# Optimization experiments

Hardware: AMD Instinct MI355X
Metric: run time of the kernel (lower is better)

## Reference

```python
import jax, jax.numpy as jnp
import numpy as np

N = 768
C_IN = 128
C_OUT = 64
C_DGRAM = 39
C_AA = 22
C_ESM = 1280
LN_EPS = 1e-5


def _layer_norm(x, g, b):
    mu = jnp.mean(x, axis=-1, keepdims=True)
    var = jnp.var(x, axis=-1, keepdims=True)
    return (x - mu) * jax.lax.rsqrt(var + LN_EPS) * g + b


def setup_inputs() -> dict:
    key = jax.random.key(0)
    ks = jax.random.split(key, 36)
    rn = lambda k, s, sc=1.0: jax.random.normal(k, s, dtype=jnp.float32) * sc
    ru = lambda k, s: jax.random.uniform(k, s, dtype=jnp.float32)
    w = lambda k, cin: rn(k, (cin, C_OUT), 1.0 / np.sqrt(cin))
    z = jnp.zeros((C_OUT,), jnp.float32)
    return {
        "template_dgram": rn(ks[0], (N, N, C_DGRAM)),
        "aatype_one_hot": ru(ks[1], (N, C_AA)),
        "query_embedding": rn(ks[2], (N, N, C_IN)),
        "pseudo_beta_mask": ru(ks[3], (N,)),
        "backbone_mask": ru(ks[4], (N,)),
        "multichain_mask_2d": ru(ks[5], (N, N)),
        "unit_x": rn(ks[6], (N, N)),
        "unit_y": rn(ks[7], (N, N)),
        "unit_z": rn(ks[8], (N, N)),
        "esm_embedding": rn(ks[9], (N, C_ESM)),
        "w_dgram": w(ks[10], C_DGRAM), "b_dgram": z,
        "w_aa1": w(ks[11], C_AA), "b_aa1": z,
        "w_aa2": w(ks[12], C_AA), "b_aa2": z,
        "ln_g": jnp.ones((C_IN,), jnp.float32), "ln_b": jnp.zeros((C_IN,), jnp.float32),
        "w_q": w(ks[13], C_IN), "b_q": z,
        "w_pbm": w(ks[14], 1), "b_pbm": z,
        "w_x": w(ks[15], 1), "b_x": z,
        "w_y": w(ks[16], 1), "b_y": z,
        "w_z": w(ks[17], 1), "b_z": z,
        "w_bb": w(ks[18], 1), "b_bb": z,
        "w_esm1": w(ks[19], C_ESM), "b_esm1": z,
        "w_esm2": w(ks[20], C_ESM), "b_esm2": z,
    }


def reference(template_dgram, aatype_one_hot, query_embedding, pseudo_beta_mask,
              backbone_mask, multichain_mask_2d, unit_x, unit_y, unit_z, esm_embedding,
              w_dgram, b_dgram, w_aa1, b_aa1, w_aa2, b_aa2, ln_g, ln_b, w_q, b_q,
              w_pbm, b_pbm, w_x, b_x, w_y, b_y, w_z, b_z, w_bb, b_bb,
              w_esm1, b_esm1, w_esm2, b_esm2):
    # pair masks [N, N]
    pb2 = pseudo_beta_mask[:, None] * pseudo_beta_mask[None, :] * multichain_mask_2d
    bb2 = backbone_mask[:, None] * backbone_mask[None, :] * multichain_mask_2d
    # masked distogram -> GEMM over bins
    act = jnp.einsum('ijd,do->ijo', template_dgram * bb2[..., None], w_dgram) + b_dgram
    # Linear(1, c_out) branches: scalar * weight row + bias (broadcasts)
    act = act + (pb2[..., None] * w_pbm[0] + b_pbm)
    # per-residue aatype projections broadcast over rows / columns
    act = act + (aatype_one_hot @ w_aa1 + b_aa1)[None, :, :]
    act = act + (aatype_one_hot @ w_aa2 + b_aa2)[:, None, :]
    act = act + ((unit_x * bb2)[..., None] * w_x[0] + b_x)
    act = act + ((unit_y * bb2)[..., None] * w_y[0] + b_y)
    act = act + ((unit_z * bb2)[..., None] * w_z[0] + b_z)
    act = act + (bb2[..., None] * w_bb[0] + b_bb)
    # per-residue ESM projections broadcast over rows / columns
    act = act + (esm_embedding @ w_esm1 + b_esm1)[None, :, :]
    act = act + (esm_embedding @ w_esm2 + b_esm2)[:, None, :]
    # LayerNorm + projection of the query pair embedding [N, N, c_in]
    q = _layer_norm(query_embedding, ln_g, ln_b)
    act = act + jnp.einsum('ijc,co->ijo', q, w_q) + b_q
    return act
```

## Files before the change

kernel.cpp:

```cpp
#include <hip/hip_runtime.h>

#define NN 768
#define CIN 128
#define COUT 64
#define CDG 39
#define CAA 22
#define CESM 1280

typedef __attribute__((ext_vector_type(8))) short short8;
typedef __attribute__((ext_vector_type(4))) float f32x4;

__device__ __forceinline__ unsigned short f2bf(float f) {
  union { float f; unsigned int i; } c; c.f = f;
  unsigned int u = c.i;
  u += 0x7fffu + ((u >> 16) & 1u);
  return (unsigned short)(u >> 16);
}
__device__ __forceinline__ unsigned int pk(float a, float b) {
  return (unsigned int)f2bf(a) | ((unsigned int)f2bf(b) << 16);
}

struct Args {
  const float *td, *aa, *q, *pbm, *bbm, *mc, *ux, *uy, *uz, *esm;
  const float *w_dgram, *b_dgram, *w_aa1, *b_aa1, *w_aa2, *b_aa2;
  const float *ln_g, *ln_b, *w_q, *b_q;
  const float *w_pbm, *b_pbm, *w_x, *b_x, *w_y, *b_y, *w_z, *b_z, *w_bb, *b_bb;
  const float *w_esm1, *b_esm1, *w_esm2, *b_esm2;
  float* out;
  float* row_vec; float* col_vec; unsigned short* b_pack;
};

__global__ __launch_bounds__(256) void k_pre(Args a) {
  const int b = blockIdx.x;
  const int tid = threadIdx.x;
  if (b == NN) {
    for (int e = tid; e < 12288; e += 256) {
      int jj = e & 7;
      int lane = (e >> 3) & 63;
      int qt = e >> 9;
      int q = qt >> 2, t = qt & 3;
      int k = q * 32 + ((lane >> 4) << 3) + jj;
      int n = t * 16 + (lane & 15);
      float v = 0.f;
      if (k < CIN) v = a.ln_g[k] * a.w_q[k * COUT + n];
      else if (k < CIN + CDG) v = a.w_dgram[(k - CIN) * COUT + n];
      else if (k == 167) v = a.w_pbm[n];
      else if (k == 168) v = a.w_x[n];
      else if (k == 169) v = a.w_y[n];
      else if (k == 170) v = a.w_z[n];
      else if (k == 171) v = a.w_bb[n];
      a.b_pack[e] = f2bf(v);
    }
    return;
  }
  const int wv = tid >> 6, lane = tid & 63;
  float acc1 = 0.f, acc2 = 0.f;
  const int KT = CAA + CESM;
  const int SL = (KT + 3) / 4;
  int k0 = wv * SL;
  int k1 = k0 + SL; if (k1 > KT) k1 = KT;
  for (int k = k0; k < k1; ++k) {
    float v; const float *w1, *w2;
    if (k < CAA) { v = a.aa[b * CAA + k]; w1 = a.w_aa1 + k * COUT; w2 = a.w_aa2 + k * COUT; }
    else { int e = k - CAA; v = a.esm[b * CESM + e]; w1 = a.w_esm1 + e * COUT; w2 = a.w_esm2 + e * COUT; }
    acc1 += v * w1[lane];
    acc2 += v * w2[lane];
  }
  __shared__ float red1[4][64];
  __shared__ float red2[4][64];
  red1[wv][lane] = acc1; red2[wv][lane] = acc2;
  __syncthreads();
  if (wv == 0) {
    float r1 = red1[0][lane] + red1[1][lane] + red1[2][lane] + red1[3][lane];
    float r2 = red2[0][lane] + red2[1][lane] + red2[2][lane] + red2[3][lane];
    float bq = 0.f;
    for (int c = 0; c < CIN; ++c) bq += a.ln_b[c] * a.w_q[c * COUT + lane];
    float br = a.b_aa1[lane] + a.b_esm1[lane] + a.b_dgram[lane] +
               a.b_pbm[lane] + a.b_x[lane] + a.b_y[lane] +
               a.b_z[lane] + a.b_bb[lane] + a.b_q[lane] + bq;
    float bc = a.b_aa2[lane] + a.b_esm2[lane];
    a.row_vec[b * COUT + lane] = r1 + br;
    a.col_vec[b * COUT + lane] = r2 + bc;
  }
}

__global__ __launch_bounds__(256, 4) void k_main(Args a) {
  const int jt = blockIdx.x;
  const int i  = blockIdx.y;
  const int jbase = jt * 64;
  const int tid = threadIdx.x;
  const int wv = tid >> 6, lane = tid & 63;
  const int m = lane & 15, quad = lane >> 4;

  __shared__ unsigned short B_lds[12288];
  __shared__ unsigned short A2[64][72];
  __shared__ float bb2_s[64];
  __shared__ float pb2_s[64];

  const float* qrow = a.q + ((size_t)i * NN + jbase + wv * 16 + m) * CIN + quad * 8;
  float4 qv[8];
#pragma unroll
  for (int qq = 0; qq < 4; ++qq) {
    qv[2 * qq]     = *(const float4*)(qrow + qq * 32);
    qv[2 * qq + 1] = *(const float4*)(qrow + qq * 32 + 4);
  }

  if (tid < 64) {
    int j = jbase + tid;
    float mc  = a.mc[(size_t)i * NN + j];
    bb2_s[tid] = a.bbm[i] * a.bbm[j] * mc;
    pb2_s[tid] = a.pbm[i] * a.pbm[j] * mc;
  }

  {
    const int4* src = (const int4*)a.b_pack;
    int4* dst = (int4*)B_lds;
#pragma unroll
    for (int r = 0; r < 6; ++r) dst[tid + 256 * r] = src[tid + 256 * r];
  }

  float sum = 0.f, sq = 0.f;
#pragma unroll
  for (int v = 0; v < 8; ++v) {
    float4 t4 = qv[v];
    sum += t4.x + t4.y + t4.z + t4.w;
    sq  += t4.x * t4.x + t4.y * t4.y + t4.z * t4.z + t4.w * t4.w;
  }
  sum += __shfl_xor(sum, 16); sum += __shfl_xor(sum, 32);
  sq  += __shfl_xor(sq, 16);  sq  += __shfl_xor(sq, 32);
  const float mu  = sum * (1.f / 128.f);
  const float var = sq * (1.f / 128.f) - mu * mu;
  const float rs  = rsqrtf(var + 1e-5f);

  short8 af[4];
#pragma unroll
  for (int qq = 0; qq < 4; ++qq) {
    union { short8 s; unsigned int w[4]; } u;
    float4 lo = qv[2 * qq], hi = qv[2 * qq + 1];
    u.w[0] = pk((lo.x - mu) * rs, (lo.y - mu) * rs);
    u.w[1] = pk((lo.z - mu) * rs, (lo.w - mu) * rs);
    u.w[2] = pk((hi.x - mu) * rs, (hi.y - mu) * rs);
    u.w[3] = pk((hi.z - mu) * rs, (hi.w - mu) * rs);
    af[qq] = u.s;
  }

  __syncthreads();

  {
    const float* base = a.td + ((size_t)i * NN + jbase) * CDG;
    const float2* src = (const float2*)base;
    for (int w = tid; w < (64 * CDG) / 2; w += 256) {
      float2 d2 = src[w];
      int f0 = w * 2;
      int p0 = (f0 * 26887) >> 20; int d0 = f0 - p0 * CDG;
      int f1 = f0 + 1;
      int p1 = (f1 * 26887) >> 20; int d1 = f1 - p1 * CDG;
      A2[p0][d0] = f2bf(d2.x * bb2_s[p0]);
      A2[p1][d1] = f2bf(d2.y * bb2_s[p1]);
    }
  }
  if (tid < 64) {
    int p = tid;
    size_t gij = (size_t)i * NN + jbase + p;
    float bb = bb2_s[p];
    A2[p][39] = f2bf(pb2_s[p]);
    A2[p][40] = f2bf(a.ux[gij] * bb);
    A2[p][41] = f2bf(a.uy[gij] * bb);
    A2[p][42] = f2bf(a.uz[gij] * bb);
    A2[p][43] = f2bf(bb);
    unsigned int* zp = (unsigned int*)&A2[p][44];
#pragma unroll
    for (int z = 0; z < 10; ++z) zp[z] = 0;
  }
  __syncthreads();

  f32x4 acc[4];
#pragma unroll
  for (int t = 0; t < 4; ++t) { f32x4 z = {0.f, 0.f, 0.f, 0.f}; acc[t] = z; }
  const unsigned short* Bb = &B_lds[lane * 8];
#pragma unroll
  for (int qq = 0; qq < 4; ++qq) {
#pragma unroll
    for (int t = 0; t < 4; ++t) {
      short8 bfr = *(const short8*)(Bb + (qq * 4 + t) * 512);
      acc[t] = __builtin_amdgcn_mfma_f32_16x16x32_bf16(af[qq], bfr, acc[t], 0, 0, 0);
    }
  }
  const unsigned short* Ab2 = &A2[wv * 16 + m][quad * 8];
#pragma unroll
  for (int q = 4; q < 6; ++q) {
    short8 a8 = *(const short8*)(Ab2 + (q - 4) * 32);
#pragma unroll
    for (int t = 0; t < 4; ++t) {
      short8 bfr = *(const short8*)(Bb + (q * 4 + t) * 512);
      acc[t] = __builtin_amdgcn_mfma_f32_16x16x32_bf16(a8, bfr, acc[t], 0, 0, 0);
    }
  }

  const float* cvp = a.col_vec + (size_t)i * COUT;
#pragma unroll
  for (int t = 0; t < 4; ++t) {
    int n = t * 16 + m;
    float cv = cvp[n];
#pragma unroll
    for (int r = 0; r < 4; ++r) {
      int p = wv * 16 + quad * 4 + r;
      int j = jbase + p;
      float val = acc[t][r] + a.row_vec[j * COUT + n] + cv;
      a.out[((size_t)i * NN + j) * COUT + n] = val;
    }
  }
}

extern "C" void kernel_launch(void* const* d_in, const int* in_sizes, int n_in,
                              void* d_out, int out_size, void* d_ws, size_t ws_size,
                              hipStream_t stream) {
  Args a;
  a.td     = (const float*)d_in[0];
  a.aa     = (const float*)d_in[1];
  a.q      = (const float*)d_in[2];
  a.pbm    = (const float*)d_in[3];
  a.bbm    = (const float*)d_in[4];
  a.mc     = (const float*)d_in[5];
  a.ux     = (const float*)d_in[6];
  a.uy     = (const float*)d_in[7];
  a.uz     = (const float*)d_in[8];
  a.esm    = (const float*)d_in[9];
  a.w_dgram = (const float*)d_in[10]; a.b_dgram = (const float*)d_in[11];
  a.w_aa1   = (const float*)d_in[12]; a.b_aa1   = (const float*)d_in[13];
  a.w_aa2   = (const float*)d_in[14]; a.b_aa2   = (const float*)d_in[15];
  a.ln_g    = (const float*)d_in[16]; a.ln_b    = (const float*)d_in[17];
  a.w_q     = (const float*)d_in[18]; a.b_q     = (const float*)d_in[19];
  a.w_pbm   = (const float*)d_in[20]; a.b_pbm   = (const float*)d_in[21];
  a.w_x     = (const float*)d_in[22]; a.b_x     = (const float*)d_in[23];
  a.w_y     = (const float*)d_in[24]; a.b_y     = (const float*)d_in[25];
  a.w_z     = (const float*)d_in[26]; a.b_z     = (const float*)d_in[27];
  a.w_bb    = (const float*)d_in[28]; a.b_bb    = (const float*)d_in[29];
  a.w_esm1  = (const float*)d_in[30]; a.b_esm1  = (const float*)d_in[31];
  a.w_esm2  = (const float*)d_in[32]; a.b_esm2  = (const float*)d_in[33];
  a.out = (float*)d_out;
  a.row_vec = (float*)d_ws;
  a.col_vec = a.row_vec + NN * COUT;
  a.b_pack  = (unsigned short*)(a.col_vec + NN * COUT);

  hipLaunchKernelGGL(k_pre, dim3(NN + 1), dim3(256), 0, stream, a);
  hipLaunchKernelGGL(k_main, dim3(12, NN), dim3(256), 0, stream, a);
}
```

Before: 744.5 us.

## Load distogram and unit features straight into MFMA A fragments, drop LDS staging

Each lane now reads its own row's distogram bins and unit-vector and mask features from global memory and packs them directly into bf16 MFMA A operands. This replaces the shared-memory A2 staging tile and removes one __syncthreads. With less LDS in use, the launch bound is raised to allow 5 blocks per CU. The trade-off is that the per-lane global reads of the 39-float rows are strided and uncoalesced, and some values are read redundantly across quads.

```diff
diff --git a/kernel.cpp b/kernel.cpp
--- a/kernel.cpp
+++ b/kernel.cpp
@@ -84,20 +84,26 @@
   }
 }
 
-__global__ __launch_bounds__(256, 4) void k_main(Args a) {
+__global__ __launch_bounds__(256, 5) void k_main(Args a) {
   const int jt = blockIdx.x;
   const int i  = blockIdx.y;
   const int jbase = jt * 64;
   const int tid = threadIdx.x;
   const int wv = tid >> 6, lane = tid & 63;
   const int m = lane & 15, quad = lane >> 4;
+  const int arow = wv * 16 + m;
+  const int aj = jbase + arow;
 
   __shared__ unsigned short B_lds[12288];
-  __shared__ unsigned short A2[64][72];
-  __shared__ float bb2_s[64];
-  __shared__ float pb2_s[64];
-
-  const float* qrow = a.q + ((size_t)i * NN + jbase + wv * 16 + m) * CIN + quad * 8;
+
+  {
+    const int4* src = (const int4*)a.b_pack;
+    int4* dst = (int4*)B_lds;
+#pragma unroll
+    for (int r = 0; r < 6; ++r) dst[tid + 256 * r] = src[tid + 256 * r];
+  }
+
+  const float* qrow = a.q + ((size_t)i * NN + aj) * CIN + quad * 8;
   float4 qv[8];
 #pragma unroll
   for (int qq = 0; qq < 4; ++qq) {
@@ -105,18 +111,43 @@
     qv[2 * qq + 1] = *(const float4*)(qrow + qq * 32 + 4);
   }
 
-  if (tid < 64) {
-    int j = jbase + tid;
-    float mc  = a.mc[(size_t)i * NN + j];
-    bb2_s[tid] = a.bbm[i] * a.bbm[j] * mc;
-    pb2_s[tid] = a.pbm[i] * a.pbm[j] * mc;
-  }
-
+  const float mc  = a.mc[(size_t)i * NN + aj];
+  const float bb2 = a.bbm[i] * a.bbm[aj] * mc;
+  const float pb2 = a.pbm[i] * a.pbm[aj] * mc;
+
+  const float* tdr = a.td + ((size_t)i * NN + aj) * CDG;
+  float dg[8];
+#pragma unroll
+  for (int e = 0; e < 8; ++e) dg[e] = tdr[quad * 8 + e];
+
+  short8 a5;
   {
-    const int4* src = (const int4*)a.b_pack;
-    int4* dst = (int4*)B_lds;
-#pragma unroll
-    for (int r = 0; r < 6; ++r) dst[tid + 256 * r] = src[tid + 256 * r];
+    union { short8 s; unsigned int w[4]; } u;
+    u.w[0] = 0u; u.w[1] = 0u; u.w[2] = 0u; u.w[3] = 0u;
+    if (quad == 0) {
+      float d0 = tdr[32], d1 = tdr[33], d2 = tdr[34], d3 = tdr[35];
+      float d4 = tdr[36], d5 = tdr[37], d6 = tdr[38];
+      u.w[0] = pk(d0 * bb2, d1 * bb2);
+      u.w[1] = pk(d2 * bb2, d3 * bb2);
+      u.w[2] = pk(d4 * bb2, d5 * bb2);
+      u.w[3] = pk(d6 * bb2, pb2);
+    } else if (quad == 1) {
+      size_t gij = (size_t)i * NN + aj;
+      float x = a.ux[gij], y = a.uy[gij], z = a.uz[gij];
+      u.w[0] = pk(x * bb2, y * bb2);
+      u.w[1] = pk(z * bb2, bb2);
+    }
+    a5 = u.s;
+  }
+
+  short8 a4;
+  {
+    union { short8 s; unsigned int w[4]; } u;
+    u.w[0] = pk(dg[0] * bb2, dg[1] * bb2);
+    u.w[1] = pk(dg[2] * bb2, dg[3] * bb2);
+    u.w[2] = pk(dg[4] * bb2, dg[5] * bb2);
+    u.w[3] = pk(dg[6] * bb2, dg[7] * bb2);
+    a4 = u.s;
   }
 
   float sum = 0.f, sq = 0.f;
@@ -146,34 +177,6 @@
 
   __syncthreads();
 
-  {
-    const float* base = a.td + ((size_t)i * NN + jbase) * CDG;
-    const float2* src = (const float2*)base;
-    for (int w = tid; w < (64 * CDG) / 2; w += 256) {
-      float2 d2 = src[w];
-      int f0 = w * 2;
-      int p0 = (f0 * 26887) >> 20; int d0 = f0 - p0 * CDG;
-      int f1 = f0 + 1;
-      int p1 = (f1 * 26887) >> 20; int d1 = f1 - p1 * CDG;
-      A2[p0][d0] = f2bf(d2.x * bb2_s[p0]);
-      A2[p1][d1] = f2bf(d2.y * bb2_s[p1]);
-    }
-  }
-  if (tid < 64) {
-    int p = tid;
-    size_t gij = (size_t)i * NN + jbase + p;
-    float bb = bb2_s[p];
-    A2[p][39] = f2bf(pb2_s[p]);
-    A2[p][40] = f2bf(a.ux[gij] * bb);
-    A2[p][41] = f2bf(a.uy[gij] * bb);
-    A2[p][42] = f2bf(a.uz[gij] * bb);
-    A2[p][43] = f2bf(bb);
-    unsigned int* zp = (unsigned int*)&A2[p][44];
-#pragma unroll
-    for (int z = 0; z < 10; ++z) zp[z] = 0;
-  }
-  __syncthreads();
-
   f32x4 acc[4];
 #pragma unroll
   for (int t = 0; t < 4; ++t) { f32x4 z = {0.f, 0.f, 0.f, 0.f}; acc[t] = z; }
@@ -186,15 +189,15 @@
       acc[t] = __builtin_amdgcn_mfma_f32_16x16x32_bf16(af[qq], bfr, acc[t], 0, 0, 0);
     }
   }
-  const unsigned short* Ab2 = &A2[wv * 16 + m][quad * 8];
-#pragma unroll
-  for (int q = 4; q < 6; ++q) {
-    short8 a8 = *(const short8*)(Ab2 + (q - 4) * 32);
-#pragma unroll
-    for (int t = 0; t < 4; ++t) {
-      short8 bfr = *(const short8*)(Bb + (q * 4 + t) * 512);
-      acc[t] = __builtin_amdgcn_mfma_f32_16x16x32_bf16(a8, bfr, acc[t], 0, 0, 0);
-    }
+#pragma unroll
+  for (int t = 0; t < 4; ++t) {
+    short8 bfr = *(const short8*)(Bb + (4 * 4 + t) * 512);
+    acc[t] = __builtin_amdgcn_mfma_f32_16x16x32_bf16(a4, bfr, acc[t], 0, 0, 0);
+  }
+#pragma unroll
+  for (int t = 0; t < 4; ++t) {
+    short8 bfr = *(const short8*)(Bb + (5 * 4 + t) * 512);
+    acc[t] = __builtin_amdgcn_mfma_f32_16x16x32_bf16(a5, bfr, acc[t], 0, 0, 0);
   }
 
   const float* cvp = a.col_vec + (size_t)i * COUT;
```

Measured after the change: 725.8 us. 2.5% less time.
